# Optimization experiments

Hardware: AMD Instinct MI355X
Metric: run time of the kernel (lower is better)

Reference implementation:

```python
import jax, jax.numpy as jnp
import numpy as np

N, M, K, C = 32768, 16384, 8, 16
LAM = 0.1        # dist_weight_lambda
EPS = 1e-6       # torch F.pairwise_distance eps (added to the difference)


def setup_inputs() -> dict:
    key = jax.random.key(0)
    k0, k1, k2, k3, k4 = jax.random.split(key, 5)
    canon_xyz = jax.random.normal(k0, (N, 3), jnp.float32)
    pred_translation = 0.1 * jax.random.normal(k1, (N, 3), jnp.float32)
    motion_coeff = jax.random.normal(k2, (N, C), jnp.float32)
    features_dc = jax.random.normal(k3, (N, 1, 3), jnp.float32)
    # random.sample without replacement -> permutation slice
    indice = jax.random.permutation(k4, N)[:M].astype(jnp.int32)
    return {
        "canon_xyz": canon_xyz,
        "pred_translation": pred_translation,
        "motion_coeff": motion_coeff,
        "features_dc": features_dc,
        "indice": indice,
    }


def _pdist(x, y):
    # torch F.pairwise_distance(p=2): ||x - y + eps|| over last dim
    d = x - y + EPS
    return jnp.sqrt(jnp.sum(d * d, axis=-1))


def reference(canon_xyz, pred_translation, motion_coeff, features_dc, indice):
    pts = canon_xyz + pred_translation            # [N,3]
    tp = pts[indice]                              # [M,3] target_points
    tc = motion_coeff[indice]                     # [M,C] target_coeffs
    tcol = features_dc[indice]                    # [M,1,3] target_colors

    # --- knn_points: brute-force squared L2, K smallest (sorted ascending) ---
    sq = jnp.sum(tp * tp, axis=-1)                # [M]
    d2 = sq[:, None] + sq[None, :] - 2.0 * (tp @ tp.T)   # [M,M]
    neg_d, nn_idx = jax.lax.top_k(-d2, K)         # [M,K]
    deform_dists = -neg_d                         # squared dists, ascending

    sim_loss = jnp.float32(0.0)

    # --- 'surface' branch ---
    nn_points = tp[nn_idx]                        # [M,K,3] knn_gather
    mean_nn_points = nn_points.mean(axis=1)       # [M,3]
    sim_loss += _pdist(tp, mean_nn_points).mean()

    # --- 'coeff' branch ---
    coeff_nn = tc[nn_idx]                         # [M,K,C]
    color_nn = tcol.reshape(M, 3)[nn_idx]         # [M,K,3]
    color_dists = _pdist(tcol, color_nn)          # [M,1,3] vs [M,K,3] -> [M,K]
    dist_weights = jnp.exp(-LAM * deform_dists ** 2)   # [M,K]
    color_weights = jnp.exp(-LAM * color_dists ** 2)   # [M,K]
    sim = _pdist(tc[:, None, :], coeff_nn)        # l2 metric -> [M,K]
    sim = color_weights * dist_weights * sim      # color_sim=True
    sim_loss += sim.mean()

    return sim_loss
```

## Files before the change

kernel.cpp:

```cpp
#include <hip/hip_runtime.h>
#include <hip/hip_bf16.h>
#include <float.h>


#define MPTS 16384
#define KNN  8
#define CDIM 16
#define LAMW 0.1f
#define EPSV 1e-6f

#define ROWS   32
#define NSPLIT 8
#define CSPL   1024
#define NT     (CSPL/32)
#define BSTR   257

#define MED3 __builtin_amdgcn_fmed3f
typedef __attribute__((ext_vector_type(8)))  _Float16 f16x8;
typedef __attribute__((ext_vector_type(16))) float    f32x16;

__global__ __launch_bounds__(256) void k_gather(
    const float* __restrict__ canon, const float* __restrict__ trans,
    const int* __restrict__ indice, float4* __restrict__ c4,
    _Float16* __restrict__ bf16b, _Float16* __restrict__ af16b,
    float* __restrict__ acc)
{
    int t = blockIdx.x * 256 + threadIdx.x;
    if (t == 0) { acc[0] = 0.f; acc[1] = 0.f; }
    if (t < MPTS) {
        int j = indice[t];
        float x = canon[3*j+0] + trans[3*j+0];
        float y = canon[3*j+1] + trans[3*j+1];
        float z = canon[3*j+2] + trans[3*j+2];
        float sq = fmaf(x, x, fmaf(y, y, z*z));
        c4[t] = make_float4(-2.f*x, -2.f*y, -2.f*z, sq);
        f16x8 aa = {};
        aa[0] = (_Float16)(-2.f*x); aa[1] = (_Float16)(-2.f*y);
        aa[2] = (_Float16)(-2.f*z); aa[3] = (_Float16)1.0f;
        *(f16x8*)(af16b + (size_t)t*8) = aa;
        f16x8 bb = {};
        bb[0] = (_Float16)x; bb[1] = (_Float16)y; bb[2] = (_Float16)z;
        bb[3] = (_Float16)sq;
        *(f16x8*)(bf16b + (size_t)t*8) = bb;
    }
}

__global__ __launch_bounds__(512, 4) void k_knn(
    const _Float16* __restrict__ bf16b, const _Float16* __restrict__ af16b,
    float* __restrict__ keys)
{
    __shared__ float bins[ROWS * BSTR];

    const int tid  = threadIdx.x;
    const int lane = tid & 63;
    const int wv   = tid >> 6;
    const int half = blockIdx.x & 1;
    const int rowbase = (blockIdx.x >> 1) * ROWS;
    const int cls  = lane & 31;
    const int cbeg = half * (MPTS/2) + wv * CSPL;

    f16x8 afrag = *(const f16x8*)(af16b + (size_t)(rowbase + cls) * 8);
    if (lane >= 32) { f16x8 zz = {}; afrag = zz; }
    f32x16 zero16 = {};

    const _Float16* bptr  = bf16b + (size_t)(cbeg + cls) * 8;
    const unsigned  HMASK = 0xFFFFC000u;
    const unsigned  ivb   = (unsigned)(cbeg + cls);

    float e0=FLT_MAX,e1=FLT_MAX,e2=FLT_MAX,e3=FLT_MAX;
    float e4=FLT_MAX,e5=FLT_MAX,e6=FLT_MAX,e7=FLT_MAX;
    float e8=FLT_MAX,e9=FLT_MAX,e10=FLT_MAX,e11=FLT_MAX;
    float e12=FLT_MAX,e13=FLT_MAX,e14=FLT_MAX,e15=FLT_MAX;

#define LD(T) (*(const f16x8*)(bptr + (size_t)(((T) & (NT-1)) * 256)))
#define DOTILE(PB, T)                                                          \
    {                                                                          \
        f32x16 dv = __builtin_amdgcn_mfma_f32_32x32x16_f16(afrag, PB, zero16, 0, 0, 0); \
        unsigned iv = ivb + (unsigned)((T) * 32);                              \
        float kf;                                                              \
        kf = __uint_as_float((__float_as_uint(dv[0])  & HMASK) | iv); e0  = fminf(e0,  kf); \
        kf = __uint_as_float((__float_as_uint(dv[1])  & HMASK) | iv); e1  = fminf(e1,  kf); \
        kf = __uint_as_float((__float_as_uint(dv[2])  & HMASK) | iv); e2  = fminf(e2,  kf); \
        kf = __uint_as_float((__float_as_uint(dv[3])  & HMASK) | iv); e3  = fminf(e3,  kf); \
        kf = __uint_as_float((__float_as_uint(dv[4])  & HMASK) | iv); e4  = fminf(e4,  kf); \
        kf = __uint_as_float((__float_as_uint(dv[5])  & HMASK) | iv); e5  = fminf(e5,  kf); \
        kf = __uint_as_float((__float_as_uint(dv[6])  & HMASK) | iv); e6  = fminf(e6,  kf); \
        kf = __uint_as_float((__float_as_uint(dv[7])  & HMASK) | iv); e7  = fminf(e7,  kf); \
        kf = __uint_as_float((__float_as_uint(dv[8])  & HMASK) | iv); e8  = fminf(e8,  kf); \
        kf = __uint_as_float((__float_as_uint(dv[9])  & HMASK) | iv); e9  = fminf(e9,  kf); \
        kf = __uint_as_float((__float_as_uint(dv[10]) & HMASK) | iv); e10 = fminf(e10, kf); \
        kf = __uint_as_float((__float_as_uint(dv[11]) & HMASK) | iv); e11 = fminf(e11, kf); \
        kf = __uint_as_float((__float_as_uint(dv[12]) & HMASK) | iv); e12 = fminf(e12, kf); \
        kf = __uint_as_float((__float_as_uint(dv[13]) & HMASK) | iv); e13 = fminf(e13, kf); \
        kf = __uint_as_float((__float_as_uint(dv[14]) & HMASK) | iv); e14 = fminf(e14, kf); \
        kf = __uint_as_float((__float_as_uint(dv[15]) & HMASK) | iv); e15 = fminf(e15, kf); \
    }

    f16x8 p0 = LD(0), p1 = LD(1), p2 = LD(2), p3 = LD(3);
    #pragma unroll
    for (int t = 0; t < NT; t += 4) {
        f16x8 n0 = LD(t+4), n1 = LD(t+5);
        DOTILE(p0, t+0)
        DOTILE(p1, t+1)
        f16x8 n2 = LD(t+6), n3 = LD(t+7);
        DOTILE(p2, t+2)
        DOTILE(p3, t+3)
        p0 = n0; p1 = n1; p2 = n2; p3 = n3;
    }
#undef DOTILE
#undef LD

    {
        float* bb = &bins[((lane >> 5) * 4) * BSTR + wv * 32 + cls];
#define ST(RO, EG) bb[(RO) * BSTR] = EG;
        ST(0,e0)   ST(1,e1)   ST(2,e2)   ST(3,e3)
        ST(8,e4)   ST(9,e5)   ST(10,e6)  ST(11,e7)
        ST(16,e8)  ST(17,e9)  ST(18,e10) ST(19,e11)
        ST(24,e12) ST(25,e13) ST(26,e14) ST(27,e15)
#undef ST
    }
    __syncthreads();

    const int sr = lane >> 4;
    const int lr = lane & 15;
    const int rl = wv * 4 + sr;
    const int row = rowbase + rl;

    float g0 = FLT_MAX, g1 = FLT_MAX;
    #pragma unroll
    for (int i = 0; i < 16; ++i) {
        float v = bins[rl * BSTR + i * 16 + lr];
        g1 = MED3(g0, g1, v);
        g0 = fminf(g0, v);
    }

    float kres = FLT_MAX;
    #pragma unroll
    for (int s = 0; s < KNN; ++s) {
        float m = g0;
        m = fminf(m, __shfl_xor(m, 1));
        m = fminf(m, __shfl_xor(m, 2));
        m = fminf(m, __shfl_xor(m, 4));
        m = fminf(m, __shfl_xor(m, 8));
        bool mine = (g0 == m);
        kres = (lr == s) ? m : kres;
        g0 = mine ? g1 : g0;
        g1 = mine ? FLT_MAX : g1;
    }

    if (lr < KNN)
        keys[((size_t)half * MPTS + row) * KNN + lr] = kres;
}

__global__ __launch_bounds__(128) void k_merge_loss(
    const float4* __restrict__ c4, const float* __restrict__ keys,
    const int* __restrict__ indice, const float* __restrict__ motion,
    const float* __restrict__ fdc, float* __restrict__ acc)
{
    __shared__ float rS[2], rM[2];
    const int tid  = threadIdx.x;
    const int lane = tid & 63;
    const int wv   = tid >> 6;
    const int row  = blockIdx.x * 128 + tid;

    const float4* pa4 = (const float4*)(keys + (size_t)row * KNN);
    const float4* pb4 = (const float4*)(keys + ((size_t)MPTS + row) * KNN);
    float4 A0 = pa4[0], A1 = pa4[1], B0 = pb4[0], B1 = pb4[1];
    float a0=A0.x,a1=A0.y,a2=A0.z,a3=A0.w,a4=A1.x,a5=A1.y,a6=A1.z,a7=A1.w;
    float b0=B0.x,b1=B0.y,b2=B0.z,b3=B0.w,b4=B1.x,b5=B1.y,b6=B1.z,b7=B1.w;

    float4 rc = c4[row];
    const float qx=-0.5f*rc.x, qy=-0.5f*rc.y, qz=-0.5f*rc.z, qq=rc.w;
    const int irow = indice[row];
    const float f0 = fdc[3*irow+0], f1 = fdc[3*irow+1], f2 = fdc[3*irow+2];
    const float4* mr4 = (const float4*)(motion + CDIM * irow);
    float4 m0 = mr4[0], m1 = mr4[1], m2 = mr4[2], m3 = mr4[3];

    float sx = 0.f, sy = 0.f, sz = 0.f, simsum = 0.f;
    #pragma unroll
    for (int s = 0; s < KNN; ++s) {
        bool m = (a0 <= b0);
        float kk = m ? a0 : b0;
        float na0=m?a1:a0, na1=m?a2:a1, na2=m?a3:a2, na3=m?a4:a3;
        float na4=m?a5:a4, na5=m?a6:a5, na6=m?a7:a6, na7=m?FLT_MAX:a7;
        float nb0=m?b0:b1, nb1=m?b1:b2, nb2=m?b2:b3, nb3=m?b3:b4;
        float nb4=m?b4:b5, nb5=m?b5:b6, nb6=m?b6:b7, nb7=m?b7:FLT_MAX;
        a0=na0;a1=na1;a2=na2;a3=na3;a4=na4;a5=na5;a6=na6;a7=na7;
        b0=nb0;b1=nb1;b2=nb2;b3=nb3;b4=nb4;b5=nb5;b6=nb6;b7=nb7;

        int jk = (int)(__float_as_uint(kk) & 0x3FFFu);
        float4 nc = c4[jk];
        float te  = fmaf(qx, nc.x, fmaf(qy, nc.y, fmaf(qz, nc.z, nc.w)));
        float d2k = qq + te;
        sx += -0.5f*nc.x; sy += -0.5f*nc.y; sz += -0.5f*nc.z;

        int inb = indice[jk];
        float c0v = f0 - fdc[3*inb+0] + EPSV;
        float c1v = f1 - fdc[3*inb+1] + EPSV;
        float c2v = f2 - fdc[3*inb+2] + EPSV;
        float cd2 = fmaf(c0v, c0v, fmaf(c1v, c1v, c2v * c2v));
        float w = __expf(-LAMW * fmaf(d2k, d2k, cd2));

        const float4* mn4 = (const float4*)(motion + CDIM * inb);
        float4 u0 = mn4[0], u1 = mn4[1], u2 = mn4[2], u3 = mn4[3];
        float sacc = 0.f;
#define MD(A,B) { float g0v=A.x-B.x+EPSV, g1v=A.y-B.y+EPSV,               \
                        g2v=A.z-B.z+EPSV, g3v=A.w-B.w+EPSV;               \
                  sacc = fmaf(g0v,g0v,fmaf(g1v,g1v,fmaf(g2v,g2v,fmaf(g3v,g3v,sacc)))); }
        MD(m0,u0) MD(m1,u1) MD(m2,u2) MD(m3,u3)
#undef MD
        simsum += w * sqrtf(sacc);
    }

    float dx = qx - sx * 0.125f + EPSV;
    float dy = qy - sy * 0.125f + EPSV;
    float dz = qz - sz * 0.125f + EPSV;
    float surf = sqrtf(fmaf(dx, dx, fmaf(dy, dy, dz * dz)));

    float aS = surf, aM = simsum;
    #pragma unroll
    for (int m = 1; m <= 32; m <<= 1) {
        aS += __shfl_xor(aS, m);
        aM += __shfl_xor(aM, m);
    }
    if (lane == 0) { rS[wv] = aS; rM[wv] = aM; }
    __syncthreads();
    if (tid == 0) {
        float tS = rS[0] + rS[1], tM = rM[0] + rM[1];
        atomicAdd(&acc[0], tS);
        atomicAdd(&acc[1], tM);
    }
}

__global__ void k_final(const float* __restrict__ acc, float* __restrict__ out)
{
    out[0] = acc[0] * (1.0f / MPTS) + acc[1] * (1.0f / (MPTS * KNN));
}

extern "C" void kernel_launch(void* const* d_in, const int* in_sizes, int n_in,
                              void* d_out, int out_size, void* d_ws, size_t ws_size,
                              hipStream_t stream)
{
    const float* canon  = (const float*)d_in[0];
    const float* trans  = (const float*)d_in[1];
    const float* motion = (const float*)d_in[2];
    const float* fdc    = (const float*)d_in[3];
    const int*   indice = (const int*)d_in[4];
    float* out = (float*)d_out;

    char* ws = (char*)d_ws;
    float*     acc   = (float*)ws;
    float4*    c4    = (float4*)(ws + 4096);
    _Float16*  af16b = (_Float16*)(ws + 4096 + 262144);
    _Float16*  bf16b = (_Float16*)(ws + 4096 + 2*262144);
    float*     keys  = (float*)(ws + 4096 + 3*262144);

    k_gather<<<MPTS/256, 256, 0, stream>>>(canon, trans, indice, c4, bf16b, af16b, acc);
    k_knn<<<(MPTS/ROWS)*2, 512, 0, stream>>>(bf16b, af16b, keys);
    k_merge_loss<<<MPTS/128, 128, 0, stream>>>(c4, keys, indice, motion, fdc, acc);
    k_final<<<1, 1, 0, stream>>>(acc, out);
}
```

Baseline: 39.72 us.

## Merge four MFMA tiles per min-reduction, resolve winning tile by exact recompute

The inner KNN loop now issues four MFMAs and takes an element-wise min across them before the index-tagging and running-min update. This cuts the per-element VALU tag/min work by roughly a factor of four. The stored candidate index now points only to the first tile of the quad, so the refine stage reloads the four candidate points 32 apart, recomputes their distances and keeps the closest. This adds gathers and arithmetic in the epilogue. It can also lose true neighbors when two of the top candidates fall in the same quad and position. The outer loop is also no longer marked for unrolling.

```diff
diff --git a/kernel.cpp b/kernel.cpp
--- a/kernel.cpp
+++ b/kernel.cpp
@@ -67,57 +67,41 @@
     const unsigned  HMASK = 0xFFFFC000u;
     const unsigned  ivb   = (unsigned)(cbeg + cls);
 
-    float e0=FLT_MAX,e1=FLT_MAX,e2=FLT_MAX,e3=FLT_MAX;
-    float e4=FLT_MAX,e5=FLT_MAX,e6=FLT_MAX,e7=FLT_MAX;
-    float e8=FLT_MAX,e9=FLT_MAX,e10=FLT_MAX,e11=FLT_MAX;
-    float e12=FLT_MAX,e13=FLT_MAX,e14=FLT_MAX,e15=FLT_MAX;
-
-#define LD(T) (*(const f16x8*)(bptr + (size_t)(((T) & (NT-1)) * 256)))
-#define DOTILE(PB, T)                                                          \
-    {                                                                          \
-        f32x16 dv = __builtin_amdgcn_mfma_f32_32x32x16_f16(afrag, PB, zero16, 0, 0, 0); \
-        unsigned iv = ivb + (unsigned)((T) * 32);                              \
-        float kf;                                                              \
-        kf = __uint_as_float((__float_as_uint(dv[0])  & HMASK) | iv); e0  = fminf(e0,  kf); \
-        kf = __uint_as_float((__float_as_uint(dv[1])  & HMASK) | iv); e1  = fminf(e1,  kf); \
-        kf = __uint_as_float((__float_as_uint(dv[2])  & HMASK) | iv); e2  = fminf(e2,  kf); \
-        kf = __uint_as_float((__float_as_uint(dv[3])  & HMASK) | iv); e3  = fminf(e3,  kf); \
-        kf = __uint_as_float((__float_as_uint(dv[4])  & HMASK) | iv); e4  = fminf(e4,  kf); \
-        kf = __uint_as_float((__float_as_uint(dv[5])  & HMASK) | iv); e5  = fminf(e5,  kf); \
-        kf = __uint_as_float((__float_as_uint(dv[6])  & HMASK) | iv); e6  = fminf(e6,  kf); \
-        kf = __uint_as_float((__float_as_uint(dv[7])  & HMASK) | iv); e7  = fminf(e7,  kf); \
-        kf = __uint_as_float((__float_as_uint(dv[8])  & HMASK) | iv); e8  = fminf(e8,  kf); \
-        kf = __uint_as_float((__float_as_uint(dv[9])  & HMASK) | iv); e9  = fminf(e9,  kf); \
-        kf = __uint_as_float((__float_as_uint(dv[10]) & HMASK) | iv); e10 = fminf(e10, kf); \
-        kf = __uint_as_float((__float_as_uint(dv[11]) & HMASK) | iv); e11 = fminf(e11, kf); \
-        kf = __uint_as_float((__float_as_uint(dv[12]) & HMASK) | iv); e12 = fminf(e12, kf); \
-        kf = __uint_as_float((__float_as_uint(dv[13]) & HMASK) | iv); e13 = fminf(e13, kf); \
-        kf = __uint_as_float((__float_as_uint(dv[14]) & HMASK) | iv); e14 = fminf(e14, kf); \
-        kf = __uint_as_float((__float_as_uint(dv[15]) & HMASK) | iv); e15 = fminf(e15, kf); \
-    }
+    float e[16];
+    #pragma unroll
+    for (int i = 0; i < 16; ++i) e[i] = FLT_MAX;
+
+    auto LD = [&](int T) -> f16x8 {
+        return *(const f16x8*)(bptr + (size_t)((T & (NT-1)) * 256));
+    };
+    auto DOQUAD = [&](f16x8 pa, f16x8 pb, f16x8 pc, f16x8 pd, int T) {
+        f32x16 dvA = __builtin_amdgcn_mfma_f32_32x32x16_f16(afrag, pa, zero16, 0, 0, 0);
+        f32x16 dvB = __builtin_amdgcn_mfma_f32_32x32x16_f16(afrag, pb, zero16, 0, 0, 0);
+        f32x16 dvC = __builtin_amdgcn_mfma_f32_32x32x16_f16(afrag, pc, zero16, 0, 0, 0);
+        f32x16 dvD = __builtin_amdgcn_mfma_f32_32x32x16_f16(afrag, pd, zero16, 0, 0, 0);
+        unsigned iv = ivb + (unsigned)(T * 32);
+        #pragma unroll
+        for (int i = 0; i < 16; ++i) {
+            float mm = fminf(fminf(dvA[i], dvB[i]), fminf(dvC[i], dvD[i]));
+            float kf = __uint_as_float((__float_as_uint(mm) & HMASK) | iv);
+            e[i] = fminf(e[i], kf);
+        }
+    };
 
     f16x8 p0 = LD(0), p1 = LD(1), p2 = LD(2), p3 = LD(3);
-    #pragma unroll
     for (int t = 0; t < NT; t += 4) {
-        f16x8 n0 = LD(t+4), n1 = LD(t+5);
-        DOTILE(p0, t+0)
-        DOTILE(p1, t+1)
-        f16x8 n2 = LD(t+6), n3 = LD(t+7);
-        DOTILE(p2, t+2)
-        DOTILE(p3, t+3)
+        f16x8 n0 = LD(t+4), n1 = LD(t+5), n2 = LD(t+6), n3 = LD(t+7);
+        DOQUAD(p0, p1, p2, p3, t);
         p0 = n0; p1 = n1; p2 = n2; p3 = n3;
     }
-#undef DOTILE
-#undef LD
 
     {
         float* bb = &bins[((lane >> 5) * 4) * BSTR + wv * 32 + cls];
-#define ST(RO, EG) bb[(RO) * BSTR] = EG;
-        ST(0,e0)   ST(1,e1)   ST(2,e2)   ST(3,e3)
-        ST(8,e4)   ST(9,e5)   ST(10,e6)  ST(11,e7)
-        ST(16,e8)  ST(17,e9)  ST(18,e10) ST(19,e11)
-        ST(24,e12) ST(25,e13) ST(26,e14) ST(27,e15)
-#undef ST
+        #pragma unroll
+        for (int g = 0; g < 16; ++g) {
+            int ro = (g & 3) + 8 * (g >> 2);
+            bb[ro * BSTR] = e[g];
+        }
     }
     __syncthreads();
 
@@ -188,10 +172,17 @@
         a0=na0;a1=na1;a2=na2;a3=na3;a4=na4;a5=na5;a6=na6;a7=na7;
         b0=nb0;b1=nb1;b2=nb2;b3=nb3;b4=nb4;b5=nb5;b6=nb6;b7=nb7;
 
-        int jk = (int)(__float_as_uint(kk) & 0x3FFFu);
-        float4 nc = c4[jk];
-        float te  = fmaf(qx, nc.x, fmaf(qy, nc.y, fmaf(qz, nc.z, nc.w)));
-        float d2k = qq + te;
+        int j0 = (int)(__float_as_uint(kk) & 0x3FFFu);
+        float4 n0 = c4[j0], n1 = c4[j0+32], n2 = c4[j0+64], n3 = c4[j0+96];
+        float d0 = qq + fmaf(qx,n0.x, fmaf(qy,n0.y, fmaf(qz,n0.z, n0.w)));
+        float d1 = qq + fmaf(qx,n1.x, fmaf(qy,n1.y, fmaf(qz,n1.z, n1.w)));
+        float d2 = qq + fmaf(qx,n2.x, fmaf(qy,n2.y, fmaf(qz,n2.z, n2.w)));
+        float d3 = qq + fmaf(qx,n3.x, fmaf(qy,n3.y, fmaf(qz,n3.z, n3.w)));
+        float d2k = d0; int jk = j0; float4 nc = n0;
+        if (d1 < d2k) { d2k = d1; jk = j0+32; nc = n1; }
+        if (d2 < d2k) { d2k = d2; jk = j0+64; nc = n2; }
+        if (d3 < d2k) { d2k = d3; jk = j0+96; nc = n3; }
+
         sx += -0.5f*nc.x; sy += -0.5f*nc.y; sz += -0.5f*nc.z;
 
         int inb = indice[jk];
```

Result: slower. 45.87 us (+15.5%).

## Parallelize merge-loss over neighbors with 16 lanes per row and rank-based merge

Applied to the files above, without the earlier changes.

The merge/loss kernel now assigns 16 lanes per query row instead of one thread per row. Each lane holds one candidate from the two KNN halves and computes its rank in the merged list by counting smaller values via shuffles. The 8 winning lanes then gather their neighbor data independently, replacing the serial 8-step merge loop and its dependent gathers. This exposes more memory-level parallelism and launches more threads, at the cost of idle lanes, redundant per-row loads, and extra shuffle reductions.

```diff
diff --git a/kernel.cpp b/kernel.cpp
--- a/kernel.cpp
+++ b/kernel.cpp
@@ -152,72 +152,81 @@
         keys[((size_t)half * MPTS + row) * KNN + lr] = kres;
 }
 
-__global__ __launch_bounds__(128) void k_merge_loss(
+__global__ __launch_bounds__(256) void k_merge_loss(
     const float4* __restrict__ c4, const float* __restrict__ keys,
     const int* __restrict__ indice, const float* __restrict__ motion,
     const float* __restrict__ fdc, float* __restrict__ acc)
 {
-    __shared__ float rS[2], rM[2];
+    __shared__ float rS[4], rM[4];
     const int tid  = threadIdx.x;
     const int lane = tid & 63;
     const int wv   = tid >> 6;
-    const int row  = blockIdx.x * 128 + tid;
-
-    const float4* pa4 = (const float4*)(keys + (size_t)row * KNN);
-    const float4* pb4 = (const float4*)(keys + ((size_t)MPTS + row) * KNN);
-    float4 A0 = pa4[0], A1 = pa4[1], B0 = pb4[0], B1 = pb4[1];
-    float a0=A0.x,a1=A0.y,a2=A0.z,a3=A0.w,a4=A1.x,a5=A1.y,a6=A1.z,a7=A1.w;
-    float b0=B0.x,b1=B0.y,b2=B0.z,b3=B0.w,b4=B1.x,b5=B1.y,b6=B1.z,b7=B1.w;
+    const int lr   = lane & 15;
+    const int row  = blockIdx.x * 16 + (tid >> 4);
+    const int base = lane & 48;
+
+    float val = (lr < KNN)
+        ? keys[(size_t)row * KNN + lr]
+        : keys[((size_t)MPTS + row) * KNN + (lr - KNN)];
+
+    int cnt = 0;
+    const int obase = base + ((lr < KNN) ? KNN : 0);
+    #pragma unroll
+    for (int j = 0; j < KNN; ++j) {
+        float o = __shfl(val, obase + j);
+        cnt += (lr < KNN) ? (o < val) : (o <= val);
+    }
+    const int rank = (lr & 7) + cnt;
+    const bool active = (rank < KNN);
 
     float4 rc = c4[row];
     const float qx=-0.5f*rc.x, qy=-0.5f*rc.y, qz=-0.5f*rc.z, qq=rc.w;
-    const int irow = indice[row];
-    const float f0 = fdc[3*irow+0], f1 = fdc[3*irow+1], f2 = fdc[3*irow+2];
-    const float4* mr4 = (const float4*)(motion + CDIM * irow);
-    float4 m0 = mr4[0], m1 = mr4[1], m2 = mr4[2], m3 = mr4[3];
-
-    float sx = 0.f, sy = 0.f, sz = 0.f, simsum = 0.f;
-    #pragma unroll
-    for (int s = 0; s < KNN; ++s) {
-        bool m = (a0 <= b0);
-        float kk = m ? a0 : b0;
-        float na0=m?a1:a0, na1=m?a2:a1, na2=m?a3:a2, na3=m?a4:a3;
-        float na4=m?a5:a4, na5=m?a6:a5, na6=m?a7:a6, na7=m?FLT_MAX:a7;
-        float nb0=m?b0:b1, nb1=m?b1:b2, nb2=m?b2:b3, nb3=m?b3:b4;
-        float nb4=m?b4:b5, nb5=m?b5:b6, nb6=m?b6:b7, nb7=m?b7:FLT_MAX;
-        a0=na0;a1=na1;a2=na2;a3=na3;a4=na4;a5=na5;a6=na6;a7=na7;
-        b0=nb0;b1=nb1;b2=nb2;b3=nb3;b4=nb4;b5=nb5;b6=nb6;b7=nb7;
-
-        int jk = (int)(__float_as_uint(kk) & 0x3FFFu);
-        float4 nc = c4[jk];
-        float te  = fmaf(qx, nc.x, fmaf(qy, nc.y, fmaf(qz, nc.z, nc.w)));
-        float d2k = qq + te;
-        sx += -0.5f*nc.x; sy += -0.5f*nc.y; sz += -0.5f*nc.z;
-
-        int inb = indice[jk];
-        float c0v = f0 - fdc[3*inb+0] + EPSV;
-        float c1v = f1 - fdc[3*inb+1] + EPSV;
-        float c2v = f2 - fdc[3*inb+2] + EPSV;
+
+    int jk = (int)(__float_as_uint(val) & 0x3FFFu);
+    float4 nc = c4[jk];
+    float te  = fmaf(qx, nc.x, fmaf(qy, nc.y, fmaf(qz, nc.z, nc.w)));
+    float d2k = qq + te;
+
+    float sx = active ? -0.5f*nc.x : 0.f;
+    float sy = active ? -0.5f*nc.y : 0.f;
+    float sz = active ? -0.5f*nc.z : 0.f;
+    sx += __shfl_xor(sx, 1); sx += __shfl_xor(sx, 2);
+    sx += __shfl_xor(sx, 4); sx += __shfl_xor(sx, 8);
+    sy += __shfl_xor(sy, 1); sy += __shfl_xor(sy, 2);
+    sy += __shfl_xor(sy, 4); sy += __shfl_xor(sy, 8);
+    sz += __shfl_xor(sz, 1); sz += __shfl_xor(sz, 2);
+    sz += __shfl_xor(sz, 4); sz += __shfl_xor(sz, 8);
+
+    float surf = 0.f, simv = 0.f;
+    if (active) {
+        if (rank == 0) {
+            float dx = qx - sx * 0.125f + EPSV;
+            float dy = qy - sy * 0.125f + EPSV;
+            float dz = qz - sz * 0.125f + EPSV;
+            surf = sqrtf(fmaf(dx, dx, fmaf(dy, dy, dz * dz)));
+        }
+        int irow = indice[row];
+        int inb  = indice[jk];
+        float c0v = fdc[3*irow+0] - fdc[3*inb+0] + EPSV;
+        float c1v = fdc[3*irow+1] - fdc[3*inb+1] + EPSV;
+        float c2v = fdc[3*irow+2] - fdc[3*inb+2] + EPSV;
         float cd2 = fmaf(c0v, c0v, fmaf(c1v, c1v, c2v * c2v));
         float w = __expf(-LAMW * fmaf(d2k, d2k, cd2));
 
+        const float4* mr4 = (const float4*)(motion + CDIM * irow);
         const float4* mn4 = (const float4*)(motion + CDIM * inb);
-        float4 u0 = mn4[0], u1 = mn4[1], u2 = mn4[2], u3 = mn4[3];
-        float sacc = 0.f;
-#define MD(A,B) { float g0v=A.x-B.x+EPSV, g1v=A.y-B.y+EPSV,               \
-                        g2v=A.z-B.z+EPSV, g3v=A.w-B.w+EPSV;               \
-                  sacc = fmaf(g0v,g0v,fmaf(g1v,g1v,fmaf(g2v,g2v,fmaf(g3v,g3v,sacc)))); }
-        MD(m0,u0) MD(m1,u1) MD(m2,u2) MD(m3,u3)
-#undef MD
-        simsum += w * sqrtf(sacc);
-    }
-
-    float dx = qx - sx * 0.125f + EPSV;
-    float dy = qy - sy * 0.125f + EPSV;
-    float dz = qz - sz * 0.125f + EPSV;
-    float surf = sqrtf(fmaf(dx, dx, fmaf(dy, dy, dz * dz)));
-
-    float aS = surf, aM = simsum;
+        float s = 0.f;
+        #pragma unroll
+        for (int c = 0; c < CDIM/4; ++c) {
+            float4 A = mr4[c], B = mn4[c];
+            float h0 = A.x-B.x+EPSV, h1 = A.y-B.y+EPSV;
+            float h2 = A.z-B.z+EPSV, h3 = A.w-B.w+EPSV;
+            s = fmaf(h0,h0, fmaf(h1,h1, fmaf(h2,h2, fmaf(h3,h3, s))));
+        }
+        simv = w * sqrtf(s);
+    }
+
+    float aS = surf, aM = simv;
     #pragma unroll
     for (int m = 1; m <= 32; m <<= 1) {
         aS += __shfl_xor(aS, m);
@@ -226,7 +235,9 @@
     if (lane == 0) { rS[wv] = aS; rM[wv] = aM; }
     __syncthreads();
     if (tid == 0) {
-        float tS = rS[0] + rS[1], tM = rM[0] + rM[1];
+        float tS = 0.f, tM = 0.f;
+        #pragma unroll
+        for (int w2 = 0; w2 < 4; ++w2) { tS += rS[w2]; tM += rM[w2]; }
         atomicAdd(&acc[0], tS);
         atomicAdd(&acc[1], tM);
     }
@@ -257,6 +268,6 @@
 
     k_gather<<<MPTS/256, 256, 0, stream>>>(canon, trans, indice, c4, bf16b, af16b, acc);
     k_knn<<<(MPTS/ROWS)*2, 512, 0, stream>>>(bf16b, af16b, keys);
-    k_merge_loss<<<MPTS/128, 128, 0, stream>>>(c4, keys, indice, motion, fdc, acc);
+    k_merge_loss<<<MPTS/16, 256, 0, stream>>>(c4, keys, indice, motion, fdc, acc);
     k_final<<<1, 1, 0, stream>>>(acc, out);
 }
```

New measurement: 61.19 us. 1.54x slower.
